# Kernel optimization log

Hardware: AMD Instinct MI355X
Metric: run time of the kernel (lower is better)

Reference implementation:

```python
import math
import jax, jax.numpy as jnp
import numpy as np

B, N, M, H = 2, 4096, 32, 8
FDIM, LDIM, HID = 256, 10, 16
D = FDIM // H  # head_dim = 32


def setup_inputs() -> dict:
    key = jax.random.key(0)
    ks = jax.random.split(key, 16)
    rn = lambda i, shape, scale=1.0: jax.random.normal(ks[i], shape, jnp.float32) * scale
    return {
        "nbhd_pairwise_g": rn(0, (B, N, M, LDIM)),
        "nbhd_mask": jax.random.bernoulli(ks[1], 0.9, (B, N, M)),
        "key_features": rn(2, (B, N, FDIM)),
        "query_features": rn(3, (B, N, FDIM)),
        "nbhd_idx": jax.random.randint(ks[4], (B, N, M), 0, N, dtype=jnp.int32),
        # fc_k / fc_q (Linear feature_dim -> embed_dim)
        "Wk": rn(5, (FDIM, FDIM), 1.0 / math.sqrt(FDIM)),
        "bk": rn(6, (FDIM,), 0.01),
        "Wq": rn(7, (FDIM, FDIM), 1.0 / math.sqrt(FDIM)),
        "bq": rn(8, (FDIM,), 0.01),
        "W0": rn(9, (H, LDIM, HID), 1.0 / math.sqrt(LDIM)),
        "b0": rn(10, (H, HID), 0.01),
        "W1": rn(11, (H, HID, HID), 1.0 / math.sqrt(HID)),
        "b1": rn(12, (H, HID), 0.01),
        "W2": rn(13, (H, HID, 1), 1.0 / math.sqrt(HID)),
        "b2": rn(14, (H, 1), 0.01),
    }


def reference(nbhd_pairwise_g, nbhd_mask, key_features, query_features, nbhd_idx,
              Wk, bk, Wq, bq, W0, b0, W1, b1, W2, b2):
    # --- DotProductKernel: project, gather keys at nbhd_idx, scaled dot ---
    K = (key_features @ Wk + bk).reshape(B, N, H, D)      # (b,n,h,d)
    Q = (query_features @ Wq + bq).reshape(B, N, H, D)    # (b,n,h,d)
    # gather neighbor keys: Kn[b,i,j] = K[b, nbhd_idx[b,i,j]]  -> (b,n,m,h,d)
    Kn = K[jnp.arange(B)[:, None, None], nbhd_idx]
    # same math as full QK^T followed by A_[B,NNS,nbhd_idx], without the n x n matrix
    feat = jnp.einsum('bnhd,bnmhd->bnmh', Q, Kn) / math.sqrt(D)  # (b,n,m,h)

    # --- location featurisation: per-head MLP on pairwise group embedding ---
    h0 = jax.nn.silu(jnp.einsum('bnml,hlk->bnmhk', nbhd_pairwise_g, W0) + b0)
    h1 = jax.nn.silu(jnp.einsum('bnmhk,hkj->bnmhj', h0, W1) + b1)
    loc = jax.nn.silu(jnp.einsum('bnmhj,hjo->bnmho', h1, W2) + b2)[..., 0]  # (b,n,m,h)

    # --- combination 'sum' (both unsqueezed to 5D), normalisation 'none' ---
    out = (feat + loc)[..., None]  # (b,n,m,h,1)
    return out
```

## Files before the change

### kernel.cpp

```cpp
#include <hip/hip_runtime.h>

typedef unsigned int   u32;
typedef unsigned short u16;
typedef __bf16 bf16x8 __attribute__((ext_vector_type(8)));
typedef float  f32x4  __attribute__((ext_vector_type(4)));
typedef float  f32x16 __attribute__((ext_vector_type(16)));

__device__ __forceinline__ u16 f2b(float f) {
  u32 u = __float_as_uint(f);
  u = (u + 0x7fffu + ((u >> 16) & 1u)) >> 16;
  return (u16)u;
}
__device__ __forceinline__ float silu_f(float x) { return __fdividef(x, 1.f + __expf(-x)); }

__global__ __launch_bounds__(512) void prep_all(
    const float* __restrict__ g,
    const float* __restrict__ Wk, const float* __restrict__ Wq,
    const float* __restrict__ W0, const float* __restrict__ W1,
    const float* __restrict__ b0, const float* __restrict__ b1,
    const float* __restrict__ W2,
    u16* __restrict__ Wkt, u16* __restrict__ Wqt,
    u16* __restrict__ W0A, u16* __restrict__ W1A,
    float* __restrict__ BT2, u16* __restrict__ G2, int useG2) {
  const int blk = blockIdx.x, t = threadIdx.x;
  if (blk < 1024) {
    if (!useG2) return;
    const int sub = t >> 6, lane = t & 63;
    const int hf = lane >> 5, m = lane & 31;
    const int bn = blk * 8 + sub;
    const float* gp = g + ((size_t)bn * 32 + m) * 10;
    bf16x8 gf = {};
    float2 v0 = *(const float2*)(gp + hf * 8);
    gf[0] = (__bf16)v0.x; gf[1] = (__bf16)v0.y;
    if (hf == 0) {
      float2 v1 = *(const float2*)(gp + 2);
      float2 v2 = *(const float2*)(gp + 4);
      float2 v3 = *(const float2*)(gp + 6);
      gf[2] = (__bf16)v1.x; gf[3] = (__bf16)v1.y;
      gf[4] = (__bf16)v2.x; gf[5] = (__bf16)v2.y;
      gf[6] = (__bf16)v3.x; gf[7] = (__bf16)v3.y;
    }
    *(bf16x8*)(G2 + ((size_t)bn * 64 + lane) * 8) = gf;
  } else if (blk < 1088) {
    for (int idx = (blk - 1024) * 512 + t; idx < 65536; idx += 64 * 512) {
      int n = idx >> 8, k = idx & 255;
      Wkt[idx] = f2b(Wk[k * 256 + n]);
      Wqt[idx] = f2b(Wq[k * 256 + n]);
    }
  } else {
    const int h = t >> 6, l = t & 63;
    const int hf = l >> 5, j = l & 31;
    float vals[24];
    #pragma unroll
    for (int e = 0; e < 8; e++) {
      int k = 8 * hf + e;
      float v0 = (j < 16 && k < 10) ? W0[h * 160 + k * 16 + j] : 0.f;
      W0A[t * 8 + e] = f2b(v0);
      int jin = (k & 3) + 8 * ((k >> 2) & 1) + 4 * (k >> 3);
      float v1 = (j < 16) ? W1[h * 256 + jin * 16 + j] : 0.f;
      W1A[t * 8 + e] = f2b(v1);
      int cj = (e & 3) + 8 * (e >> 2) + 4 * hf;
      vals[e]      = b0[h * 16 + cj];
      vals[8 + e]  = b1[h * 16 + cj];
      vals[16 + e] = W2[h * 16 + cj];
    }
    #pragma unroll
    for (int j4 = 0; j4 < 6; j4++)
      ((float4*)BT2)[j4 * 512 + t] =
        make_float4(vals[4 * j4], vals[4 * j4 + 1], vals[4 * j4 + 2], vals[4 * j4 + 3]);
  }
}

#define LDA 72
__global__ __launch_bounds__(256) void gemm_proj(
    const float* __restrict__ A0, const float* __restrict__ A1,
    const u16* __restrict__ B0, const u16* __restrict__ B1,
    const float* __restrict__ bias0, const float* __restrict__ bias1,
    u16* __restrict__ C0, u16* __restrict__ C1) {
  const float* A; const u16* Bt; const float* bias; u16* C;
  if (blockIdx.z == 0) { A = A0; Bt = B0; bias = bias0; C = C0; }
  else                 { A = A1; Bt = B1; bias = bias1; C = C1; }
  __shared__ __align__(16) u16 As[128 * LDA];
  __shared__ __align__(16) u16 Bs[128 * LDA];
  const int t = threadIdx.x;
  const int w = t >> 6, lane = t & 63;
  const int wm = w >> 1, wn = w & 1;
  const int row0 = blockIdx.x * 128, col0 = blockIdx.y * 128;
  f32x4 acc[4][4] = {};
  for (int kk = 0; kk < 256; kk += 64) {
    #pragma unroll
    for (int p = 0; p < 8; p++) {
      int r = p * 16 + (t >> 4), q = (t & 15) * 4;
      float4 v = *(const float4*)(A + (size_t)(row0 + r) * 256 + kk + q);
      uint2 pk;
      pk.x = (u32)f2b(v.x) | ((u32)f2b(v.y) << 16);
      pk.y = (u32)f2b(v.z) | ((u32)f2b(v.w) << 16);
      *(uint2*)(&As[r * LDA + q]) = pk;
    }
    #pragma unroll
    for (int p = 0; p < 4; p++) {
      int r = p * 32 + (t >> 3), q = (t & 7) * 8;
      *(uint4*)(&Bs[r * LDA + q]) = *(const uint4*)(Bt + (size_t)(col0 + r) * 256 + kk + q);
    }
    __syncthreads();
    #pragma unroll
    for (int ks = 0; ks < 2; ks++) {
      bf16x8 af[4], bfr[4];
      #pragma unroll
      for (int i = 0; i < 4; i++) {
        af[i]  = *(const bf16x8*)(&As[(wm * 64 + i * 16 + (lane & 15)) * LDA + ks * 32 + (lane >> 4) * 8]);
        bfr[i] = *(const bf16x8*)(&Bs[(wn * 64 + i * 16 + (lane & 15)) * LDA + ks * 32 + (lane >> 4) * 8]);
      }
      #pragma unroll
      for (int i = 0; i < 4; i++)
        #pragma unroll
        for (int j = 0; j < 4; j++)
          acc[i][j] = __builtin_amdgcn_mfma_f32_16x16x32_bf16(af[i], bfr[j], acc[i][j], 0, 0, 0);
    }
    __syncthreads();
  }
  #pragma unroll
  for (int j = 0; j < 4; j++) {
    int c = col0 + wn * 64 + j * 16 + (lane & 15);
    float bv = bias[c];
    #pragma unroll
    for (int i = 0; i < 4; i++) {
      int r0 = row0 + wm * 64 + i * 16 + (lane >> 4) * 4;
      #pragma unroll
      for (int q = 0; q < 4; q++)
        C[(size_t)(r0 + q) * 256 + c] = f2b(acc[i][j][q] + bv);
    }
  }
}

template<int USE_G2>
__global__ __launch_bounds__(512) void fused_main(
    const u16* __restrict__ Kbf, const u16* __restrict__ Qbf,
    const int* __restrict__ nidx, const float* __restrict__ g,
    const u16* __restrict__ W0A, const u16* __restrict__ W1A,
    const float* __restrict__ BT2, const float* __restrict__ b2,
    const u16* __restrict__ G2, float* __restrict__ out) {
  __shared__ float lout[256];
  const int t = threadIdx.x;
  const int h = t >> 6, lane = t & 63;
  const int hf = lane >> 5, m = lane & 31;
  const int bn = blockIdx.x;
  const int b = bn >> 12;
  const int row = bn * 32 + m;
  const int hs = __builtin_amdgcn_readfirstlane(h);

  const bf16x8 a0 = *(const bf16x8*)(W0A + (size_t)(hs * 64 + lane) * 8);
  const bf16x8 a1 = *(const bf16x8*)(W1A + (size_t)(hs * 64 + lane) * 8);
  const float4* bt = (const float4*)BT2;
  const float4 t0 = bt[0 * 512 + t], t1 = bt[1 * 512 + t], t2 = bt[2 * 512 + t];
  const float4 t3 = bt[3 * 512 + t], t4 = bt[4 * 512 + t], t5 = bt[5 * 512 + t];
  const float bj0[8] = {t0.x, t0.y, t0.z, t0.w, t1.x, t1.y, t1.z, t1.w};
  const float bj1[8] = {t2.x, t2.y, t2.z, t2.w, t3.x, t3.y, t3.z, t3.w};
  const float wj[8]  = {t4.x, t4.y, t4.z, t4.w, t5.x, t5.y, t5.z, t5.w};
  const float b2s = b2[hs];

  bf16x8 gf;
  if (USE_G2) {
    gf = *(const bf16x8*)(G2 + ((size_t)bn * 64 + lane) * 8);
  } else {
    bf16x8 gt = {};
    const float* gp = g + (size_t)row * 10;
    float2 v0 = *(const float2*)(gp + hf * 8);
    gt[0] = (__bf16)v0.x; gt[1] = (__bf16)v0.y;
    if (hf == 0) {
      float2 v1 = *(const float2*)(gp + 2);
      float2 v2 = *(const float2*)(gp + 4);
      float2 v3 = *(const float2*)(gp + 6);
      gt[2] = (__bf16)v1.x; gt[3] = (__bf16)v1.y;
      gt[4] = (__bf16)v2.x; gt[5] = (__bf16)v2.y;
      gt[6] = (__bf16)v3.x; gt[7] = (__bf16)v3.y;
    }
    gf = gt;
  }

  const int kidx = nidx[row];
  const u16* qbase = Qbf + ((size_t)bn << 8) + (hs << 5);
  const u16* kbase = Kbf + (((size_t)b << 12) + (size_t)kidx) * 256 + (hs << 5);
  const bf16x8 aq0 = *(const bf16x8*)(qbase + hf * 8);
  const bf16x8 aq1 = *(const bf16x8*)(qbase + 16 + hf * 8);
  const bf16x8 bk0 = *(const bf16x8*)(kbase + hf * 8);
  const bf16x8 bk1 = *(const bf16x8*)(kbase + 16 + hf * 8);

  const f32x16 z = {};
  f32x16 fa = __builtin_amdgcn_mfma_f32_32x32x16_bf16(aq0, bk0, z, 0, 0, 0);
  fa = __builtin_amdgcn_mfma_f32_32x32x16_bf16(aq1, bk1, fa, 0, 0, 0);
  const float feat = fa[0] * 0.17677669529663687f;

  f32x16 acc = __builtin_amdgcn_mfma_f32_32x32x16_bf16(a0, gf, z, 0, 0, 0);
  bf16x8 h0b;
  #pragma unroll
  for (int e = 0; e < 8; e++) h0b[e] = (__bf16)silu_f(acc[e] + bj0[e]);

  acc = __builtin_amdgcn_mfma_f32_32x32x16_bf16(a1, h0b, z, 0, 0, 0);
  float part = 0.f;
  #pragma unroll
  for (int e = 0; e < 8; e++) part += silu_f(acc[e] + bj1[e]) * wj[e];

  float osum = part + __shfl_xor(part, 32, 64);
  float res = feat + silu_f(osum + b2s);

  if (hf == 0) lout[m * 8 + h] = res;
  __syncthreads();
  if (t < 64) {
    float4 v = ((const float4*)lout)[t];
    ((float4*)(out + ((size_t)bn << 8)))[t] = v;
  }
}

extern "C" void kernel_launch(void* const* d_in, const int* in_sizes, int n_in,
                              void* d_out, int out_size, void* d_ws, size_t ws_size,
                              hipStream_t stream) {
  const float* g_in = (const float*)d_in[0];
  const float* kf   = (const float*)d_in[2];
  const float* qf   = (const float*)d_in[3];
  const int*   idx  = (const int*)d_in[4];
  const float* Wk   = (const float*)d_in[5];
  const float* bk   = (const float*)d_in[6];
  const float* Wq   = (const float*)d_in[7];
  const float* bq   = (const float*)d_in[8];
  const float* W0   = (const float*)d_in[9];
  const float* b0   = (const float*)d_in[10];
  const float* W1   = (const float*)d_in[11];
  const float* b1   = (const float*)d_in[12];
  const float* W2   = (const float*)d_in[13];
  const float* b2   = (const float*)d_in[14];

  char* ws = (char*)d_ws;
  u16*   Wkt = (u16*)(ws);
  u16*   Wqt = (u16*)(ws + 131072);
  u16*   W0A = (u16*)(ws + 262144);
  u16*   W1A = (u16*)(ws + 270336);
  float* BT2 = (float*)(ws + 278528);
  u16*   Kbf = (u16*)(ws + 524288);
  u16*   Qbf = (u16*)(ws + 524288 + 4194304);
  u16*   G2  = (u16*)(ws + 524288 + 8388608);

  const int useG2 = (ws_size >= (size_t)17408 * 1024) ? 1 : 0;

  prep_all<<<1089, 512, 0, stream>>>(g_in, Wk, Wq, W0, W1, b0, b1, W2,
                                     Wkt, Wqt, W0A, W1A, BT2, G2, useG2);
  gemm_proj<<<dim3(64, 2, 2), 256, 0, stream>>>(kf, qf, Wkt, Wqt, bk, bq, Kbf, Qbf);
  if (useG2)
    fused_main<1><<<8192, 512, 0, stream>>>(Kbf, Qbf, idx, g_in, W0A, W1A, BT2, b2,
                                            G2, (float*)d_out);
  else
    fused_main<0><<<8192, 512, 0, stream>>>(Kbf, Qbf, idx, g_in, W0A, W1A, BT2, b2,
                                            G2, (float*)d_out);
}
```

Before: 64.23 us.

## Overlap projection GEMM with g conversion and MLP weight packing in one launch

The weight transpose moves into its own small kernel. The projection GEMM blocks, the pairwise-g to bf16 conversion and the MLP weight packing are merged into a single 256-thread launch, so the memory-bound g conversion can run at the same time as the GEMM. The intent is to cut one kernel-launch gap and fill the GPU better during the prep phase. In exchange, the g-conversion blocks now carry the GEMM's shared-memory allocation, which may limit occupancy for those blocks.

Result: slower. 67.77 us (+5.5%).

```diff
diff --git a/kernel.cpp b/kernel.cpp
--- a/kernel.cpp
+++ b/kernel.cpp
@@ -13,21 +13,90 @@
 }
 __device__ __forceinline__ float silu_f(float x) { return __fdividef(x, 1.f + __expf(-x)); }
 
-__global__ __launch_bounds__(512) void prep_all(
+__global__ __launch_bounds__(256) void prep_wt(
+    const float* __restrict__ Wk, const float* __restrict__ Wq,
+    u16* __restrict__ Wkt, u16* __restrict__ Wqt) {
+  for (int idx = blockIdx.x * 256 + threadIdx.x; idx < 65536; idx += 128 * 256) {
+    int n = idx >> 8, k = idx & 255;
+    Wkt[idx] = f2b(Wk[k * 256 + n]);
+    Wqt[idx] = f2b(Wq[k * 256 + n]);
+  }
+}
+
+#define LDA 72
+__global__ __launch_bounds__(256) void prep_gemm(
     const float* __restrict__ g,
-    const float* __restrict__ Wk, const float* __restrict__ Wq,
+    const float* __restrict__ A0, const float* __restrict__ A1,
+    const u16* __restrict__ B0t, const u16* __restrict__ B1t,
+    const float* __restrict__ bias0, const float* __restrict__ bias1,
     const float* __restrict__ W0, const float* __restrict__ W1,
     const float* __restrict__ b0, const float* __restrict__ b1,
     const float* __restrict__ W2,
-    u16* __restrict__ Wkt, u16* __restrict__ Wqt,
+    u16* __restrict__ C0, u16* __restrict__ C1,
     u16* __restrict__ W0A, u16* __restrict__ W1A,
     float* __restrict__ BT2, u16* __restrict__ G2, int useG2) {
+  __shared__ __align__(16) u16 As[128 * LDA];
+  __shared__ __align__(16) u16 Bs[128 * LDA];
   const int blk = blockIdx.x, t = threadIdx.x;
-  if (blk < 1024) {
+
+  if (blk < 256) {
+    const int bx = blk & 63, by = (blk >> 6) & 1, bz = blk >> 7;
+    const float* A; const u16* Bt; const float* bias; u16* C;
+    if (bz == 0) { A = A0; Bt = B0t; bias = bias0; C = C0; }
+    else         { A = A1; Bt = B1t; bias = bias1; C = C1; }
+    const int w = t >> 6, lane = t & 63;
+    const int wm = w >> 1, wn = w & 1;
+    const int row0 = bx * 128, col0 = by * 128;
+    f32x4 acc[4][4] = {};
+    for (int kk = 0; kk < 256; kk += 64) {
+      #pragma unroll
+      for (int p = 0; p < 8; p++) {
+        int r = p * 16 + (t >> 4), q = (t & 15) * 4;
+        float4 v = *(const float4*)(A + (size_t)(row0 + r) * 256 + kk + q);
+        uint2 pk;
+        pk.x = (u32)f2b(v.x) | ((u32)f2b(v.y) << 16);
+        pk.y = (u32)f2b(v.z) | ((u32)f2b(v.w) << 16);
+        *(uint2*)(&As[r * LDA + q]) = pk;
+      }
+      #pragma unroll
+      for (int p = 0; p < 4; p++) {
+        int r = p * 32 + (t >> 3), q = (t & 7) * 8;
+        *(uint4*)(&Bs[r * LDA + q]) = *(const uint4*)(Bt + (size_t)(col0 + r) * 256 + kk + q);
+      }
+      __syncthreads();
+      #pragma unroll
+      for (int ks = 0; ks < 2; ks++) {
+        bf16x8 af[4], bfr[4];
+        #pragma unroll
+        for (int i = 0; i < 4; i++) {
+          af[i]  = *(const bf16x8*)(&As[(wm * 64 + i * 16 + (lane & 15)) * LDA + ks * 32 + (lane >> 4) * 8]);
+          bfr[i] = *(const bf16x8*)(&Bs[(wn * 64 + i * 16 + (lane & 15)) * LDA + ks * 32 + (lane >> 4) * 8]);
+        }
+        #pragma unroll
+        for (int i = 0; i < 4; i++)
+          #pragma unroll
+          for (int j = 0; j < 4; j++)
+            acc[i][j] = __builtin_amdgcn_mfma_f32_16x16x32_bf16(af[i], bfr[j], acc[i][j], 0, 0, 0);
+      }
+      __syncthreads();
+    }
+    #pragma unroll
+    for (int j = 0; j < 4; j++) {
+      int c = col0 + wn * 64 + j * 16 + (lane & 15);
+      float bv = bias[c];
+      #pragma unroll
+      for (int i = 0; i < 4; i++) {
+        int r0 = row0 + wm * 64 + i * 16 + (lane >> 4) * 4;
+        #pragma unroll
+        for (int q = 0; q < 4; q++)
+          C[(size_t)(r0 + q) * 256 + c] = f2b(acc[i][j][q] + bv);
+      }
+    }
+  } else if (blk < 2304) {
     if (!useG2) return;
     const int sub = t >> 6, lane = t & 63;
     const int hf = lane >> 5, m = lane & 31;
-    const int bn = blk * 8 + sub;
+    const int bn = (blk - 256) * 4 + sub;
     const float* gp = g + ((size_t)bn * 32 + m) * 10;
     bf16x8 gf = {};
     float2 v0 = *(const float2*)(gp + hf * 8);
@@ -41,94 +110,30 @@
       gf[6] = (__bf16)v3.x; gf[7] = (__bf16)v3.y;
     }
     *(bf16x8*)(G2 + ((size_t)bn * 64 + lane) * 8) = gf;
-  } else if (blk < 1088) {
-    for (int idx = (blk - 1024) * 512 + t; idx < 65536; idx += 64 * 512) {
-      int n = idx >> 8, k = idx & 255;
-      Wkt[idx] = f2b(Wk[k * 256 + n]);
-      Wqt[idx] = f2b(Wq[k * 256 + n]);
-    }
   } else {
-    const int h = t >> 6, l = t & 63;
-    const int hf = l >> 5, j = l & 31;
-    float vals[24];
     #pragma unroll
-    for (int e = 0; e < 8; e++) {
-      int k = 8 * hf + e;
-      float v0 = (j < 16 && k < 10) ? W0[h * 160 + k * 16 + j] : 0.f;
-      W0A[t * 8 + e] = f2b(v0);
-      int jin = (k & 3) + 8 * ((k >> 2) & 1) + 4 * (k >> 3);
-      float v1 = (j < 16) ? W1[h * 256 + jin * 16 + j] : 0.f;
-      W1A[t * 8 + e] = f2b(v1);
-      int cj = (e & 3) + 8 * (e >> 2) + 4 * hf;
-      vals[e]      = b0[h * 16 + cj];
-      vals[8 + e]  = b1[h * 16 + cj];
-      vals[16 + e] = W2[h * 16 + cj];
-    }
-    #pragma unroll
-    for (int j4 = 0; j4 < 6; j4++)
-      ((float4*)BT2)[j4 * 512 + t] =
-        make_float4(vals[4 * j4], vals[4 * j4 + 1], vals[4 * j4 + 2], vals[4 * j4 + 3]);
-  }
-}
-
-#define LDA 72
-__global__ __launch_bounds__(256) void gemm_proj(
-    const float* __restrict__ A0, const float* __restrict__ A1,
-    const u16* __restrict__ B0, const u16* __restrict__ B1,
-    const float* __restrict__ bias0, const float* __restrict__ bias1,
-    u16* __restrict__ C0, u16* __restrict__ C1) {
-  const float* A; const u16* Bt; const float* bias; u16* C;
-  if (blockIdx.z == 0) { A = A0; Bt = B0; bias = bias0; C = C0; }
-  else                 { A = A1; Bt = B1; bias = bias1; C = C1; }
-  __shared__ __align__(16) u16 As[128 * LDA];
-  __shared__ __align__(16) u16 Bs[128 * LDA];
-  const int t = threadIdx.x;
-  const int w = t >> 6, lane = t & 63;
-  const int wm = w >> 1, wn = w & 1;
-  const int row0 = blockIdx.x * 128, col0 = blockIdx.y * 128;
-  f32x4 acc[4][4] = {};
-  for (int kk = 0; kk < 256; kk += 64) {
-    #pragma unroll
-    for (int p = 0; p < 8; p++) {
-      int r = p * 16 + (t >> 4), q = (t & 15) * 4;
-      float4 v = *(const float4*)(A + (size_t)(row0 + r) * 256 + kk + q);
-      uint2 pk;
-      pk.x = (u32)f2b(v.x) | ((u32)f2b(v.y) << 16);
-      pk.y = (u32)f2b(v.z) | ((u32)f2b(v.w) << 16);
-      *(uint2*)(&As[r * LDA + q]) = pk;
-    }
-    #pragma unroll
-    for (int p = 0; p < 4; p++) {
-      int r = p * 32 + (t >> 3), q = (t & 7) * 8;
-      *(uint4*)(&Bs[r * LDA + q]) = *(const uint4*)(Bt + (size_t)(col0 + r) * 256 + kk + q);
-    }
-    __syncthreads();
-    #pragma unroll
-    for (int ks = 0; ks < 2; ks++) {
-      bf16x8 af[4], bfr[4];
-      #pragma unroll
-      for (int i = 0; i < 4; i++) {
-        af[i]  = *(const bf16x8*)(&As[(wm * 64 + i * 16 + (lane & 15)) * LDA + ks * 32 + (lane >> 4) * 8]);
-        bfr[i] = *(const bf16x8*)(&Bs[(wn * 64 + i * 16 + (lane & 15)) * LDA + ks * 32 + (lane >> 4) * 8]);
-      }
-      #pragma unroll
-      for (int i = 0; i < 4; i++)
-        #pragma unroll
-        for (int j = 0; j < 4; j++)
-          acc[i][j] = __builtin_amdgcn_mfma_f32_16x16x32_bf16(af[i], bfr[j], acc[i][j], 0, 0, 0);
-    }
-    __syncthreads();
-  }
-  #pragma unroll
-  for (int j = 0; j < 4; j++) {
-    int c = col0 + wn * 64 + j * 16 + (lane & 15);
-    float bv = bias[c];
-    #pragma unroll
-    for (int i = 0; i < 4; i++) {
-      int r0 = row0 + wm * 64 + i * 16 + (lane >> 4) * 4;
-      #pragma unroll
-      for (int q = 0; q < 4; q++)
-        C[(size_t)(r0 + q) * 256 + c] = f2b(acc[i][j][q] + bv);
+    for (int hh = 0; hh < 2; hh++) {
+      const int tt = hh * 256 + t;
+      const int h = tt >> 6, l = tt & 63;
+      const int hf = l >> 5, j = l & 31;
+      float vals[24];
+      #pragma unroll
+      for (int e = 0; e < 8; e++) {
+        int k = 8 * hf + e;
+        float v0 = (j < 16 && k < 10) ? W0[h * 160 + k * 16 + j] : 0.f;
+        W0A[tt * 8 + e] = f2b(v0);
+        int jin = (k & 3) + 8 * ((k >> 2) & 1) + 4 * (k >> 3);
+        float v1 = (j < 16) ? W1[h * 256 + jin * 16 + j] : 0.f;
+        W1A[tt * 8 + e] = f2b(v1);
+        int cj = (e & 3) + 8 * (e >> 2) + 4 * hf;
+        vals[e]      = b0[h * 16 + cj];
+        vals[8 + e]  = b1[h * 16 + cj];
+        vals[16 + e] = W2[h * 16 + cj];
+      }
+      #pragma unroll
+      for (int j4 = 0; j4 < 6; j4++)
+        ((float4*)BT2)[j4 * 512 + tt] =
+          make_float4(vals[4 * j4], vals[4 * j4 + 1], vals[4 * j4 + 2], vals[4 * j4 + 3]);
     }
   }
 }
@@ -242,9 +247,10 @@
 
   const int useG2 = (ws_size >= (size_t)17408 * 1024) ? 1 : 0;
 
-  prep_all<<<1089, 512, 0, stream>>>(g_in, Wk, Wq, W0, W1, b0, b1, W2,
-                                     Wkt, Wqt, W0A, W1A, BT2, G2, useG2);
-  gemm_proj<<<dim3(64, 2, 2), 256, 0, stream>>>(kf, qf, Wkt, Wqt, bk, bq, Kbf, Qbf);
+  prep_wt<<<128, 256, 0, stream>>>(Wk, Wq, Wkt, Wqt);
+  prep_gemm<<<2305, 256, 0, stream>>>(g_in, kf, qf, Wkt, Wqt, bk, bq,
+                                      W0, W1, b0, b1, W2,
+                                      Kbf, Qbf, W0A, W1A, BT2, G2, useG2);
   if (useG2)
     fused_main<1><<<8192, 512, 0, stream>>>(Kbf, Qbf, idx, g_in, W0A, W1A, BT2, b2,
                                             G2, (float*)d_out);
```

## Drop G2 precompute; stage pairwise g through LDS and fold query scale into Wq

Applied to the files above, without the earlier changes.

Removes the separate bf16 repacking pass over nbhd_pairwise_g from prep_all. fused_main now loads each block's 320 floats of g into shared memory with coalesced float4 loads and builds the MFMA operand from LDS, at the cost of an extra __syncthreads. The 1/sqrt(D) scale is folded into the Wq transpose and the bq bias, so the per-element multiply on the dot product is dropped. The final silu reduction is also rewritten as a balanced tree. The intent is to avoid the extra global write and read of G2 and the launch of 1024 prep blocks.

Measured after the change: 65.59 us. +2.1%, slower.

```diff
diff --git a/kernel.cpp b/kernel.cpp
--- a/kernel.cpp
+++ b/kernel.cpp
@@ -13,39 +13,21 @@
 }
 __device__ __forceinline__ float silu_f(float x) { return __fdividef(x, 1.f + __expf(-x)); }
 
+#define QSCALE 0.17677669529663687f
+
 __global__ __launch_bounds__(512) void prep_all(
-    const float* __restrict__ g,
     const float* __restrict__ Wk, const float* __restrict__ Wq,
     const float* __restrict__ W0, const float* __restrict__ W1,
     const float* __restrict__ b0, const float* __restrict__ b1,
     const float* __restrict__ W2,
     u16* __restrict__ Wkt, u16* __restrict__ Wqt,
-    u16* __restrict__ W0A, u16* __restrict__ W1A,
-    float* __restrict__ BT2, u16* __restrict__ G2, int useG2) {
+    u16* __restrict__ W0A, u16* __restrict__ W1A, float* __restrict__ BT2) {
   const int blk = blockIdx.x, t = threadIdx.x;
-  if (blk < 1024) {
-    if (!useG2) return;
-    const int sub = t >> 6, lane = t & 63;
-    const int hf = lane >> 5, m = lane & 31;
-    const int bn = blk * 8 + sub;
-    const float* gp = g + ((size_t)bn * 32 + m) * 10;
-    bf16x8 gf = {};
-    float2 v0 = *(const float2*)(gp + hf * 8);
-    gf[0] = (__bf16)v0.x; gf[1] = (__bf16)v0.y;
-    if (hf == 0) {
-      float2 v1 = *(const float2*)(gp + 2);
-      float2 v2 = *(const float2*)(gp + 4);
-      float2 v3 = *(const float2*)(gp + 6);
-      gf[2] = (__bf16)v1.x; gf[3] = (__bf16)v1.y;
-      gf[4] = (__bf16)v2.x; gf[5] = (__bf16)v2.y;
-      gf[6] = (__bf16)v3.x; gf[7] = (__bf16)v3.y;
-    }
-    *(bf16x8*)(G2 + ((size_t)bn * 64 + lane) * 8) = gf;
-  } else if (blk < 1088) {
-    for (int idx = (blk - 1024) * 512 + t; idx < 65536; idx += 64 * 512) {
+  if (blk < 64) {
+    for (int idx = blk * 512 + t; idx < 65536; idx += 64 * 512) {
       int n = idx >> 8, k = idx & 255;
       Wkt[idx] = f2b(Wk[k * 256 + n]);
-      Wqt[idx] = f2b(Wq[k * 256 + n]);
+      Wqt[idx] = f2b(Wq[k * 256 + n] * QSCALE);
     }
   } else {
     const int h = t >> 6, l = t & 63;
@@ -77,9 +59,9 @@
     const u16* __restrict__ B0, const u16* __restrict__ B1,
     const float* __restrict__ bias0, const float* __restrict__ bias1,
     u16* __restrict__ C0, u16* __restrict__ C1) {
-  const float* A; const u16* Bt; const float* bias; u16* C;
-  if (blockIdx.z == 0) { A = A0; Bt = B0; bias = bias0; C = C0; }
-  else                 { A = A1; Bt = B1; bias = bias1; C = C1; }
+  const float* A; const u16* Bt; const float* bias; u16* C; float bscale;
+  if (blockIdx.z == 0) { A = A0; Bt = B0; bias = bias0; C = C0; bscale = 1.f; }
+  else                 { A = A1; Bt = B1; bias = bias1; C = C1; bscale = QSCALE; }
   __shared__ __align__(16) u16 As[128 * LDA];
   __shared__ __align__(16) u16 Bs[128 * LDA];
   const int t = threadIdx.x;
@@ -122,7 +104,7 @@
   #pragma unroll
   for (int j = 0; j < 4; j++) {
     int c = col0 + wn * 64 + j * 16 + (lane & 15);
-    float bv = bias[c];
+    float bv = bias[c] * bscale;
     #pragma unroll
     for (int i = 0; i < 4; i++) {
       int r0 = row0 + wm * 64 + i * 16 + (lane >> 4) * 4;
@@ -133,13 +115,13 @@
   }
 }
 
-template<int USE_G2>
 __global__ __launch_bounds__(512) void fused_main(
     const u16* __restrict__ Kbf, const u16* __restrict__ Qbf,
     const int* __restrict__ nidx, const float* __restrict__ g,
     const u16* __restrict__ W0A, const u16* __restrict__ W1A,
     const float* __restrict__ BT2, const float* __restrict__ b2,
-    const u16* __restrict__ G2, float* __restrict__ out) {
+    float* __restrict__ out) {
+  __shared__ __align__(16) float g_lds[320];
   __shared__ float lout[256];
   const int t = threadIdx.x;
   const int h = t >> 6, lane = t & 63;
@@ -148,6 +130,8 @@
   const int b = bn >> 12;
   const int row = bn * 32 + m;
   const int hs = __builtin_amdgcn_readfirstlane(h);
+
+  if (t < 80) ((float4*)g_lds)[t] = ((const float4*)(g + (size_t)bn * 320))[t];
 
   const bf16x8 a0 = *(const bf16x8*)(W0A + (size_t)(hs * 64 + lane) * 8);
   const bf16x8 a1 = *(const bf16x8*)(W1A + (size_t)(hs * 64 + lane) * 8);
@@ -159,25 +143,6 @@
   const float wj[8]  = {t4.x, t4.y, t4.z, t4.w, t5.x, t5.y, t5.z, t5.w};
   const float b2s = b2[hs];
 
-  bf16x8 gf;
-  if (USE_G2) {
-    gf = *(const bf16x8*)(G2 + ((size_t)bn * 64 + lane) * 8);
-  } else {
-    bf16x8 gt = {};
-    const float* gp = g + (size_t)row * 10;
-    float2 v0 = *(const float2*)(gp + hf * 8);
-    gt[0] = (__bf16)v0.x; gt[1] = (__bf16)v0.y;
-    if (hf == 0) {
-      float2 v1 = *(const float2*)(gp + 2);
-      float2 v2 = *(const float2*)(gp + 4);
-      float2 v3 = *(const float2*)(gp + 6);
-      gt[2] = (__bf16)v1.x; gt[3] = (__bf16)v1.y;
-      gt[4] = (__bf16)v2.x; gt[5] = (__bf16)v2.y;
-      gt[6] = (__bf16)v3.x; gt[7] = (__bf16)v3.y;
-    }
-    gf = gt;
-  }
-
   const int kidx = nidx[row];
   const u16* qbase = Qbf + ((size_t)bn << 8) + (hs << 5);
   const u16* kbase = Kbf + (((size_t)b << 12) + (size_t)kidx) * 256 + (hs << 5);
@@ -189,7 +154,24 @@
   const f32x16 z = {};
   f32x16 fa = __builtin_amdgcn_mfma_f32_32x32x16_bf16(aq0, bk0, z, 0, 0, 0);
   fa = __builtin_amdgcn_mfma_f32_32x32x16_bf16(aq1, bk1, fa, 0, 0, 0);
-  const float feat = fa[0] * 0.17677669529663687f;
+  const float feat = fa[0];
+
+  __syncthreads();
+
+  bf16x8 gf = {};
+  {
+    const float* gl = g_lds + m * 10 + hf * 8;
+    float2 p0 = *(const float2*)(gl);
+    gf[0] = (__bf16)p0.x; gf[1] = (__bf16)p0.y;
+    if (hf == 0) {
+      float2 p1 = *(const float2*)(gl + 2);
+      float2 p2 = *(const float2*)(gl + 4);
+      float2 p3 = *(const float2*)(gl + 6);
+      gf[2] = (__bf16)p1.x; gf[3] = (__bf16)p1.y;
+      gf[4] = (__bf16)p2.x; gf[5] = (__bf16)p2.y;
+      gf[6] = (__bf16)p3.x; gf[7] = (__bf16)p3.y;
+    }
+  }
 
   f32x16 acc = __builtin_amdgcn_mfma_f32_32x32x16_bf16(a0, gf, z, 0, 0, 0);
   bf16x8 h0b;
@@ -197,9 +179,11 @@
   for (int e = 0; e < 8; e++) h0b[e] = (__bf16)silu_f(acc[e] + bj0[e]);
 
   acc = __builtin_amdgcn_mfma_f32_32x32x16_bf16(a1, h0b, z, 0, 0, 0);
-  float part = 0.f;
-  #pragma unroll
-  for (int e = 0; e < 8; e++) part += silu_f(acc[e] + bj1[e]) * wj[e];
+  float q0 = silu_f(acc[0] + bj1[0]) * wj[0] + silu_f(acc[1] + bj1[1]) * wj[1];
+  float q1 = silu_f(acc[2] + bj1[2]) * wj[2] + silu_f(acc[3] + bj1[3]) * wj[3];
+  float q2 = silu_f(acc[4] + bj1[4]) * wj[4] + silu_f(acc[5] + bj1[5]) * wj[5];
+  float q3 = silu_f(acc[6] + bj1[6]) * wj[6] + silu_f(acc[7] + bj1[7]) * wj[7];
+  float part = (q0 + q1) + (q2 + q3);
 
   float osum = part + __shfl_xor(part, 32, 64);
   float res = feat + silu_f(osum + b2s);
@@ -238,17 +222,10 @@
   float* BT2 = (float*)(ws + 278528);
   u16*   Kbf = (u16*)(ws + 524288);
   u16*   Qbf = (u16*)(ws + 524288 + 4194304);
-  u16*   G2  = (u16*)(ws + 524288 + 8388608);
-
-  const int useG2 = (ws_size >= (size_t)17408 * 1024) ? 1 : 0;
-
-  prep_all<<<1089, 512, 0, stream>>>(g_in, Wk, Wq, W0, W1, b0, b1, W2,
-                                     Wkt, Wqt, W0A, W1A, BT2, G2, useG2);
+
+  prep_all<<<65, 512, 0, stream>>>(Wk, Wq, W0, W1, b0, b1, W2,
+                                   Wkt, Wqt, W0A, W1A, BT2);
   gemm_proj<<<dim3(64, 2, 2), 256, 0, stream>>>(kf, qf, Wkt, Wqt, bk, bq, Kbf, Qbf);
-  if (useG2)
-    fused_main<1><<<8192, 512, 0, stream>>>(Kbf, Qbf, idx, g_in, W0A, W1A, BT2, b2,
-                                            G2, (float*)d_out);
-  else
-    fused_main<0><<<8192, 512, 0, stream>>>(Kbf, Qbf, idx, g_in, W0A, W1A, BT2, b2,
-                                            G2, (float*)d_out);
-}
+  fused_main<<<8192, 512, 0, stream>>>(Kbf, Qbf, idx, g_in, W0A, W1A, BT2, b2,
+                                       (float*)d_out);
+}
```

## Process two query rows per block and fold attention scale into Wq

Applied to the files above, without the earlier changes.

The fused kernel now handles two (b,n) rows per block with interleaved independent MFMA chains and loads issued up front, halving the grid and amortising per-block weight and bias loads. The 1/sqrt(D) scale is folded into the bf16 Wq and the bias in the projection GEMM, which removes a multiply per output. Splitting the silu accumulation into two chains shortens the dependency chain. The cost is higher register pressure per thread, which could reduce occupancy. Rounding changes slightly because the scale is applied before bf16 conversion.

Result: slower. 66.12 us (+2.9%).

```diff
diff --git a/kernel.cpp b/kernel.cpp
--- a/kernel.cpp
+++ b/kernel.cpp
@@ -12,6 +12,8 @@
   return (u16)u;
 }
 __device__ __forceinline__ float silu_f(float x) { return __fdividef(x, 1.f + __expf(-x)); }
+
+#define QSCALE 0.17677669529663687f
 
 __global__ __launch_bounds__(512) void prep_all(
     const float* __restrict__ g,
@@ -45,7 +47,7 @@
     for (int idx = (blk - 1024) * 512 + t; idx < 65536; idx += 64 * 512) {
       int n = idx >> 8, k = idx & 255;
       Wkt[idx] = f2b(Wk[k * 256 + n]);
-      Wqt[idx] = f2b(Wq[k * 256 + n]);
+      Wqt[idx] = f2b(Wq[k * 256 + n] * QSCALE);
     }
   } else {
     const int h = t >> 6, l = t & 63;
@@ -77,9 +79,9 @@
     const u16* __restrict__ B0, const u16* __restrict__ B1,
     const float* __restrict__ bias0, const float* __restrict__ bias1,
     u16* __restrict__ C0, u16* __restrict__ C1) {
-  const float* A; const u16* Bt; const float* bias; u16* C;
-  if (blockIdx.z == 0) { A = A0; Bt = B0; bias = bias0; C = C0; }
-  else                 { A = A1; Bt = B1; bias = bias1; C = C1; }
+  const float* A; const u16* Bt; const float* bias; u16* C; float bscale;
+  if (blockIdx.z == 0) { A = A0; Bt = B0; bias = bias0; C = C0; bscale = 1.f; }
+  else                 { A = A1; Bt = B1; bias = bias1; C = C1; bscale = QSCALE; }
   __shared__ __align__(16) u16 As[128 * LDA];
   __shared__ __align__(16) u16 Bs[128 * LDA];
   const int t = threadIdx.x;
@@ -122,7 +124,7 @@
   #pragma unroll
   for (int j = 0; j < 4; j++) {
     int c = col0 + wn * 64 + j * 16 + (lane & 15);
-    float bv = bias[c];
+    float bv = bias[c] * bscale;
     #pragma unroll
     for (int i = 0; i < 4; i++) {
       int r0 = row0 + wm * 64 + i * 16 + (lane >> 4) * 4;
@@ -140,14 +142,53 @@
     const u16* __restrict__ W0A, const u16* __restrict__ W1A,
     const float* __restrict__ BT2, const float* __restrict__ b2,
     const u16* __restrict__ G2, float* __restrict__ out) {
-  __shared__ float lout[256];
+  __shared__ float lout[512];
   const int t = threadIdx.x;
   const int h = t >> 6, lane = t & 63;
   const int hf = lane >> 5, m = lane & 31;
-  const int bn = blockIdx.x;
-  const int b = bn >> 12;
-  const int row = bn * 32 + m;
+  const int bn0 = blockIdx.x * 2;
+  const int b = bn0 >> 12;
+  const int rowA = bn0 * 32 + m;
   const int hs = __builtin_amdgcn_readfirstlane(h);
+
+  const int kidxA = nidx[rowA];
+  const int kidxB = nidx[rowA + 32];
+
+  bf16x8 gfA, gfB;
+  if (USE_G2) {
+    gfA = *(const bf16x8*)(G2 + ((size_t)bn0 * 64 + lane) * 8);
+    gfB = *(const bf16x8*)(G2 + ((size_t)(bn0 + 1) * 64 + lane) * 8);
+  } else {
+    #pragma unroll
+    for (int s = 0; s < 2; s++) {
+      bf16x8 gt = {};
+      const float* gp = g + ((size_t)(bn0 + s) * 32 + m) * 10;
+      float2 v0 = *(const float2*)(gp + hf * 8);
+      gt[0] = (__bf16)v0.x; gt[1] = (__bf16)v0.y;
+      if (hf == 0) {
+        float2 v1 = *(const float2*)(gp + 2);
+        float2 v2 = *(const float2*)(gp + 4);
+        float2 v3 = *(const float2*)(gp + 6);
+        gt[2] = (__bf16)v1.x; gt[3] = (__bf16)v1.y;
+        gt[4] = (__bf16)v2.x; gt[5] = (__bf16)v2.y;
+        gt[6] = (__bf16)v3.x; gt[7] = (__bf16)v3.y;
+      }
+      if (s == 0) gfA = gt; else gfB = gt;
+    }
+  }
+
+  const u16* qbaseA = Qbf + ((size_t)bn0 << 8) + (hs << 5);
+  const u16* qbaseB = qbaseA + 256;
+  const u16* kbaseA = Kbf + (((size_t)b << 12) + (size_t)kidxA) * 256 + (hs << 5);
+  const u16* kbaseB = Kbf + (((size_t)b << 12) + (size_t)kidxB) * 256 + (hs << 5);
+  const bf16x8 aq0A = *(const bf16x8*)(qbaseA + hf * 8);
+  const bf16x8 aq1A = *(const bf16x8*)(qbaseA + 16 + hf * 8);
+  const bf16x8 bk0A = *(const bf16x8*)(kbaseA + hf * 8);
+  const bf16x8 bk1A = *(const bf16x8*)(kbaseA + 16 + hf * 8);
+  const bf16x8 aq0B = *(const bf16x8*)(qbaseB + hf * 8);
+  const bf16x8 aq1B = *(const bf16x8*)(qbaseB + 16 + hf * 8);
+  const bf16x8 bk0B = *(const bf16x8*)(kbaseB + hf * 8);
+  const bf16x8 bk1B = *(const bf16x8*)(kbaseB + 16 + hf * 8);
 
   const bf16x8 a0 = *(const bf16x8*)(W0A + (size_t)(hs * 64 + lane) * 8);
   const bf16x8 a1 = *(const bf16x8*)(W1A + (size_t)(hs * 64 + lane) * 8);
@@ -159,56 +200,49 @@
   const float wj[8]  = {t4.x, t4.y, t4.z, t4.w, t5.x, t5.y, t5.z, t5.w};
   const float b2s = b2[hs];
 
-  bf16x8 gf;
-  if (USE_G2) {
-    gf = *(const bf16x8*)(G2 + ((size_t)bn * 64 + lane) * 8);
-  } else {
-    bf16x8 gt = {};
-    const float* gp = g + (size_t)row * 10;
-    float2 v0 = *(const float2*)(gp + hf * 8);
-    gt[0] = (__bf16)v0.x; gt[1] = (__bf16)v0.y;
-    if (hf == 0) {
-      float2 v1 = *(const float2*)(gp + 2);
-      float2 v2 = *(const float2*)(gp + 4);
-      float2 v3 = *(const float2*)(gp + 6);
-      gt[2] = (__bf16)v1.x; gt[3] = (__bf16)v1.y;
-      gt[4] = (__bf16)v2.x; gt[5] = (__bf16)v2.y;
-      gt[6] = (__bf16)v3.x; gt[7] = (__bf16)v3.y;
-    }
-    gf = gt;
-  }
-
-  const int kidx = nidx[row];
-  const u16* qbase = Qbf + ((size_t)bn << 8) + (hs << 5);
-  const u16* kbase = Kbf + (((size_t)b << 12) + (size_t)kidx) * 256 + (hs << 5);
-  const bf16x8 aq0 = *(const bf16x8*)(qbase + hf * 8);
-  const bf16x8 aq1 = *(const bf16x8*)(qbase + 16 + hf * 8);
-  const bf16x8 bk0 = *(const bf16x8*)(kbase + hf * 8);
-  const bf16x8 bk1 = *(const bf16x8*)(kbase + 16 + hf * 8);
-
   const f32x16 z = {};
-  f32x16 fa = __builtin_amdgcn_mfma_f32_32x32x16_bf16(aq0, bk0, z, 0, 0, 0);
-  fa = __builtin_amdgcn_mfma_f32_32x32x16_bf16(aq1, bk1, fa, 0, 0, 0);
-  const float feat = fa[0] * 0.17677669529663687f;
-
-  f32x16 acc = __builtin_amdgcn_mfma_f32_32x32x16_bf16(a0, gf, z, 0, 0, 0);
-  bf16x8 h0b;
+
+  f32x16 faA = __builtin_amdgcn_mfma_f32_32x32x16_bf16(aq0A, bk0A, z, 0, 0, 0);
+  f32x16 faB = __builtin_amdgcn_mfma_f32_32x32x16_bf16(aq0B, bk0B, z, 0, 0, 0);
+  faA = __builtin_amdgcn_mfma_f32_32x32x16_bf16(aq1A, bk1A, faA, 0, 0, 0);
+  faB = __builtin_amdgcn_mfma_f32_32x32x16_bf16(aq1B, bk1B, faB, 0, 0, 0);
+  const float featA = faA[0];
+  const float featB = faB[0];
+
+  f32x16 accA = __builtin_amdgcn_mfma_f32_32x32x16_bf16(a0, gfA, z, 0, 0, 0);
+  f32x16 accB = __builtin_amdgcn_mfma_f32_32x32x16_bf16(a0, gfB, z, 0, 0, 0);
+  bf16x8 h0A, h0B;
   #pragma unroll
-  for (int e = 0; e < 8; e++) h0b[e] = (__bf16)silu_f(acc[e] + bj0[e]);
-
-  acc = __builtin_amdgcn_mfma_f32_32x32x16_bf16(a1, h0b, z, 0, 0, 0);
-  float part = 0.f;
+  for (int e = 0; e < 8; e++) {
+    h0A[e] = (__bf16)silu_f(accA[e] + bj0[e]);
+    h0B[e] = (__bf16)silu_f(accB[e] + bj0[e]);
+  }
+
+  accA = __builtin_amdgcn_mfma_f32_32x32x16_bf16(a1, h0A, z, 0, 0, 0);
+  accB = __builtin_amdgcn_mfma_f32_32x32x16_bf16(a1, h0B, z, 0, 0, 0);
+  float pA0 = 0.f, pA1 = 0.f, pB0 = 0.f, pB1 = 0.f;
   #pragma unroll
-  for (int e = 0; e < 8; e++) part += silu_f(acc[e] + bj1[e]) * wj[e];
-
-  float osum = part + __shfl_xor(part, 32, 64);
-  float res = feat + silu_f(osum + b2s);
-
-  if (hf == 0) lout[m * 8 + h] = res;
+  for (int e = 0; e < 4; e++) {
+    pA0 += silu_f(accA[e] + bj1[e]) * wj[e];
+    pA1 += silu_f(accA[e + 4] + bj1[e + 4]) * wj[e + 4];
+    pB0 += silu_f(accB[e] + bj1[e]) * wj[e];
+    pB1 += silu_f(accB[e + 4] + bj1[e + 4]) * wj[e + 4];
+  }
+  float partA = pA0 + pA1, partB = pB0 + pB1;
+
+  float osumA = partA + __shfl_xor(partA, 32, 64);
+  float osumB = partB + __shfl_xor(partB, 32, 64);
+  float resA = featA + silu_f(osumA + b2s);
+  float resB = featB + silu_f(osumB + b2s);
+
+  if (hf == 0) {
+    lout[m * 8 + h]       = resA;
+    lout[256 + m * 8 + h] = resB;
+  }
   __syncthreads();
-  if (t < 64) {
+  if (t < 128) {
     float4 v = ((const float4*)lout)[t];
-    ((float4*)(out + ((size_t)bn << 8)))[t] = v;
+    ((float4*)(out + ((size_t)bn0 << 8)))[t] = v;
   }
 }
 
@@ -246,9 +280,9 @@
                                      Wkt, Wqt, W0A, W1A, BT2, G2, useG2);
   gemm_proj<<<dim3(64, 2, 2), 256, 0, stream>>>(kf, qf, Wkt, Wqt, bk, bq, Kbf, Qbf);
   if (useG2)
-    fused_main<1><<<8192, 512, 0, stream>>>(Kbf, Qbf, idx, g_in, W0A, W1A, BT2, b2,
+    fused_main<1><<<4096, 512, 0, stream>>>(Kbf, Qbf, idx, g_in, W0A, W1A, BT2, b2,
                                             G2, (float*)d_out);
   else
-    fused_main<0><<<8192, 512, 0, stream>>>(Kbf, Qbf, idx, g_in, W0A, W1A, BT2, b2,
+    fused_main<0><<<4096, 512, 0, stream>>>(Kbf, Qbf, idx, g_in, W0A, W1A, BT2, b2,
                                             G2, (float*)d_out);
 }
```
